# Kernel optimization log

Hardware: AMD Instinct MI355X
Metric: run time of the kernel (lower is better)

The kernel has to match this reference:

```python
import jax, jax.numpy as jnp
import numpy as np

B, LAT, H, F, L, NL = 128, 128, 512, 128, 256, 2


def setup_inputs() -> dict:
    key = jax.random.key(0)
    ks = jax.random.split(key, 20)
    s = 0.05  # keep recurrence well-conditioned
    def n(k, shp):
        return jax.random.normal(k, shp, dtype=jnp.float32) * s
    return dict(
        z=jax.random.normal(ks[0], (B, LAT), dtype=jnp.float32),
        W_l2h=n(ks[1], (H * NL, LAT)), b_l2h=n(ks[2], (H * NL,)),
        W_l2c=n(ks[3], (H * NL, LAT)), b_l2c=n(ks[4], (H * NL,)),
        W_zp=n(ks[5], (H, LAT)), b_zp=n(ks[6], (H,)),
        W_ih0=n(ks[7], (4 * H, F + H)), W_hh0=n(ks[8], (4 * H, H)),
        b_ih0=n(ks[9], (4 * H,)), b_hh0=n(ks[10], (4 * H,)),
        W_ih1=n(ks[11], (4 * H, H)), W_hh1=n(ks[12], (4 * H, H)),
        b_ih1=n(ks[13], (4 * H,)), b_hh1=n(ks[14], (4 * H,)),
        ln_g=jnp.ones((H,), jnp.float32), ln_b=jnp.zeros((H,), jnp.float32),
        W_pre=n(ks[15], (H, H)), b_pre=n(ks[16], (H,)),
        W_out=n(ks[17], (F, H)), b_out=n(ks[18], (F,)),
    )


def _lstm_cell(x, h, c, Wih, Whh, bih, bhh):
    # PyTorch gate order: i, f, g, o
    gates = x @ Wih.T + bih + h @ Whh.T + bhh
    i, f, g, o = jnp.split(gates, 4, axis=-1)
    c = jax.nn.sigmoid(f) * c + jax.nn.sigmoid(i) * jnp.tanh(g)
    h = jax.nn.sigmoid(o) * jnp.tanh(c)
    return h, c


def _layernorm(x, g, b, eps=1e-5):
    m = jnp.mean(x, axis=-1, keepdims=True)
    v = jnp.var(x, axis=-1, keepdims=True)
    return (x - m) * jax.lax.rsqrt(v + eps) * g + b


def reference(z, W_l2h, b_l2h, W_l2c, b_l2c, W_zp, b_zp,
              W_ih0, W_hh0, b_ih0, b_hh0, W_ih1, W_hh1, b_ih1, b_hh1,
              ln_g, ln_b, W_pre, b_pre, W_out, b_out):
    # Faithful to torch: (B, NL*H) viewed row-major as (NL, B, H)
    h0 = (z @ W_l2h.T + b_l2h).reshape(NL, B, H)
    c0 = (z @ W_l2c.T + b_l2c).reshape(NL, B, H)
    z_proj = z @ W_zp.T + b_zp  # (B, H), injected every step
    dec0 = jnp.zeros((B, F), dtype=z.dtype)

    def step(carry, _):
        ha, ca, hb, cb, dec = carry
        x = jnp.concatenate([dec, z_proj], axis=-1)  # (B, F+H)
        ha, ca = _lstm_cell(x, ha, ca, W_ih0, W_hh0, b_ih0, b_hh0)
        hb, cb = _lstm_cell(ha, hb, cb, W_ih1, W_hh1, b_ih1, b_hh1)
        ln = _layernorm(hb, ln_g, ln_b)
        pre = jax.nn.relu(ln @ W_pre.T + b_pre)
        out_t = (pre + ln) @ W_out.T + b_out  # residual through MLP
        return (ha, ca, hb, cb, out_t), out_t

    _, ys = jax.lax.scan(step, (h0[0], c0[0], h0[1], c0[1], dec0), None, length=L)
    return jnp.transpose(ys, (1, 0, 2))  # (B, L, F)
```

## Files before the change

### kernel.cpp

```cpp
#include <hip/hip_runtime.h>
#include <hip/hip_cooperative_groups.h>

namespace cg = cooperative_groups;


typedef unsigned int uint32;
typedef unsigned short u16;
typedef __attribute__((ext_vector_type(8))) short bf16x8;
typedef __attribute__((ext_vector_type(4))) float f32x4;

static constexpr int Ln = 256, Fn = 128;
static constexpr int APS = 65536;
static constexpr int WPS = 2097152;
static constexpr int OPS = 65536;
static constexpr int PPS = 262144;

static constexpr int BAR_WORDS = 4096;

static constexpr int ROWP = 520;
static constexpr int PLANE = 16 * ROWP;
static constexpr int SACT_ELEMS = 6 * PLANE;

static constexpr int SM_HV   = 0;
static constexpr int SM_LNH  = 33024;
static constexpr int SM_LNM  = 49664;
static constexpr int SM_LNL  = 66304;
static constexpr int SM_RED  = 82944;
static constexpr int SM_MEAN = 83968;
static constexpr int SM_RSTD = 84032;
static constexpr int SMEM_BYTES = 84096;

__device__ __forceinline__ u16 f2bf(float f) {
  union { float f; uint32 u; } v; v.f = f;
  uint32 u = v.u + 0x7fffu + ((v.u >> 16) & 1u);
  return (u16)(u >> 16);
}
__device__ __forceinline__ float bf2f(u16 h) {
  union { uint32 u; float f; } v; v.u = ((uint32)h) << 16;
  return v.f;
}
__device__ __forceinline__ void splitbf3(float v, u16* hi, u16* mid, u16* lo) {
  u16 h = f2bf(v);
  float r = v - bf2f(h);
  u16 m = f2bf(r);
  float r2 = r - bf2f(m);
  *hi = h; *mid = m; *lo = f2bf(r2);
}
__device__ __forceinline__ float sigm(float x) { return 1.f / (1.f + expf(-x)); }
__device__ __forceinline__ bf16x8 ldf(const u16* p) { return *(const bf16x8*)p; }

__device__ __forceinline__ bf16x8 ldc16(const u16* p) {
  bf16x8 r;
  asm volatile("global_load_dwordx4 %0, %1, off sc0 sc1" : "=v"(r) : "v"(p) : "memory");
  return r;
}
__device__ __forceinline__ void stc2(u16* p, u16 v) {
  asm volatile("global_store_short %0, %1, off sc0 sc1" :: "v"(p), "v"((uint32)v) : "memory");
}
__device__ __forceinline__ void vwait0_fence() {
  asm volatile("s_waitcnt vmcnt(0)" ::: "memory");
  __builtin_amdgcn_sched_barrier(0);
}

__device__ __forceinline__ void gbar_g(uint32* arr, uint32 ep, int blk) {
  asm volatile("s_waitcnt vmcnt(0) lgkmcnt(0)" ::: "memory");
  __syncthreads();
  int tid = threadIdx.x;
  if (tid == 0)
    __hip_atomic_store(&arr[blk * 16], ep, __ATOMIC_RELAXED, __HIP_MEMORY_SCOPE_AGENT);
  int base = (blk >> 5) << 5;
  for (;;) {
    uint32 v = (tid < 32)
        ? __hip_atomic_load(&arr[(base + tid) * 16], __ATOMIC_RELAXED, __HIP_MEMORY_SCOPE_AGENT)
        : ep;
    if (__syncthreads_and(v >= ep)) break;
    __builtin_amdgcn_s_sleep(1);
  }
  __builtin_amdgcn_sched_barrier(0);
}

#define MFMA1(A, B, ACC) ACC = __builtin_amdgcn_mfma_f32_16x16x32_bf16((A), (B), (ACC), 0, 0, 0)
#define MFMA6(AH, AM, AL, BH, BM, BL, A0, A1, A2) \
  do {                                            \
    MFMA1(AH, BH, A0);                            \
    MFMA1(AH, BM, A1); MFMA1(AM, BH, A1);         \
    MFMA1(AH, BL, A2); MFMA1(AL, BH, A2);         \
    MFMA1(AM, BM, A2);                            \
  } while (0)


__device__ __forceinline__ void stage_side(const u16* __restrict__ g, int b0,
                                           u16* sAct, int sideBase, int tid) {
  bf16x8 tv[12];
#pragma unroll
  for (int jr = 0; jr < 12; ++jr) {
    int plane = jr >> 2;
    int c2 = tid + ((jr & 3) << 8);
    int row = c2 >> 6, col = c2 & 63;
    tv[jr] = ldc16(g + (size_t)plane * APS + (size_t)(b0 + row) * 512 + col * 8);
  }
  vwait0_fence();
#pragma unroll
  for (int jr = 0; jr < 12; ++jr) {
    int plane = jr >> 2;
    int c2 = tid + ((jr & 3) << 8);
    int row = c2 >> 6, col = c2 & 63;
    *(bf16x8*)&sAct[sideBase + plane * PLANE + row * ROWP + col * 8] = tv[jr];
  }
}

__device__ __forceinline__ void gate_tile_p(
    const u16* __restrict__ g0, const u16* __restrict__ g1,
    const u16* __restrict__ wr,
    const float* __restrict__ bias, int bias_stride,
    float& cr, u16* __restrict__ hout,
    int b0, int h0, int tid, u16* sAct, float (*gbuf)[16][16]) {
  stage_side(g0, b0, sAct, 0, tid);
  stage_side(g1, b0, sAct, 3 * PLANE, tid);
  __syncthreads();
  int lane = tid & 63, w = tid >> 6, q = lane >> 4, r16 = lane & 15;
  const u16* aB = sAct + r16 * ROWP + q * 8;
  f32x4 A0 = {0.f, 0.f, 0.f, 0.f}, A1 = {0.f, 0.f, 0.f, 0.f}, A2 = {0.f, 0.f, 0.f, 0.f};
#pragma unroll
  for (int kb = 0; kb < 16; ++kb) {
    bf16x8 ah = ldf(aB + kb * 32), am = ldf(aB + PLANE + kb * 32), al = ldf(aB + 2 * PLANE + kb * 32);
    bf16x8 bh = ldf(wr + kb * 32), bm = ldf(wr + WPS + kb * 32), bl = ldf(wr + 2 * WPS + kb * 32);
    MFMA6(ah, am, al, bh, bm, bl, A0, A1, A2);
  }
#pragma unroll
  for (int kb = 0; kb < 16; ++kb) {
    bf16x8 ah = ldf(aB + 3 * PLANE + kb * 32), am = ldf(aB + 4 * PLANE + kb * 32),
           al = ldf(aB + 5 * PLANE + kb * 32);
    bf16x8 bh = ldf(wr + 512 + kb * 32), bm = ldf(wr + WPS + 512 + kb * 32),
           bl = ldf(wr + 2 * WPS + 512 + kb * 32);
    MFMA6(ah, am, al, bh, bm, bl, A0, A1, A2);
  }
#pragma unroll
  for (int r = 0; r < 4; ++r)
    gbuf[w][q * 4 + r][r16] = (A2[r] + A1[r]) + A0[r];
  __syncthreads();
  int bl_ = tid >> 4, hl = tid & 15;
  int b = b0 + bl_, h = h0 + hl;
  const float* bb = bias + (size_t)b * bias_stride;
  float gi = gbuf[0][bl_][hl] + bb[h];
  float gf = gbuf[1][bl_][hl] + bb[512 + h];
  float gc = gbuf[2][bl_][hl] + bb[1024 + h];
  float go = gbuf[3][bl_][hl] + bb[1536 + h];
  int idx = b * 512 + h;
  float cn = sigm(gf) * cr + sigm(gi) * tanhf(gc);
  cr = cn;
  float hv_ = sigm(go) * tanhf(cn);
  u16 hh, hm, hl2;
  splitbf3(hv_, &hh, &hm, &hl2);
  stc2(hout + idx, hh);
  stc2(hout + APS + idx, hm);
  stc2(hout + 2 * APS + idx, hl2);
}

__device__ __forceinline__ void ys_tile_p(
    const u16* __restrict__ sg, const u16* __restrict__ wr,
    const float* __restrict__ b_out, float* __restrict__ ys,
    int tout, int b0, int f0, int tid, u16* sAct) {
  stage_side(sg, b0, sAct, 0, tid);
  __syncthreads();
  int lane = tid & 63, q = lane >> 4, r16 = lane & 15;
  const u16* aB = sAct + r16 * ROWP + q * 8;
  f32x4 A0 = {0.f, 0.f, 0.f, 0.f}, A1 = {0.f, 0.f, 0.f, 0.f}, A2 = {0.f, 0.f, 0.f, 0.f};
#pragma unroll
  for (int kb = 0; kb < 16; ++kb) {
    bf16x8 ah = ldf(aB + kb * 32), am = ldf(aB + PLANE + kb * 32), al = ldf(aB + 2 * PLANE + kb * 32);
    bf16x8 bh = ldf(wr + kb * 32), bm = ldf(wr + OPS + kb * 32), bl = ldf(wr + 2 * OPS + kb * 32);
    MFMA6(ah, am, al, bh, bm, bl, A0, A1, A2);
  }
  int fc = f0 + r16;
  float bo = b_out[fc];
#pragma unroll
  for (int r = 0; r < 4; ++r) {
    int b = b0 + q * 4 + r;
    ys[(size_t)b * (Ln * Fn) + (size_t)tout * Fn + fc] = ((A2[r] + A1[r]) + A0[r]) + bo;
  }
}

__device__ __forceinline__ void lnpre_tile_p(
    const u16* __restrict__ hb, const u16* __restrict__ wr,
    const float* __restrict__ lng, const float* __restrict__ lnb,
    const float* __restrict__ b_pre, u16* __restrict__ s_out,
    int j0, int b0, int tid, char* smem) {
  float* hv = (float*)(smem + SM_HV);
  u16* lnH = (u16*)(smem + SM_LNH);
  u16* lnM = (u16*)(smem + SM_LNM);
  u16* lnL = (u16*)(smem + SM_LNL);
  float (*red)[16] = (float (*)[16])(smem + SM_RED);
  float* smean = (float*)(smem + SM_MEAN);
  float* srstd = (float*)(smem + SM_RSTD);
  bf16x8 p[12];
#pragma unroll
  for (int jj = 0; jj < 4; ++jj) {
    int c = tid + 256 * jj;
    int b = c >> 6, k0 = (c & 63) * 8;
    size_t base = (size_t)(b0 + b) * 512 + k0;
    p[jj * 3 + 0] = ldc16(hb + base);
    p[jj * 3 + 1] = ldc16(hb + APS + base);
    p[jj * 3 + 2] = ldc16(hb + 2 * APS + base);
  }
  vwait0_fence();
#pragma unroll
  for (int jj = 0; jj < 4; ++jj) {
    int c = tid + 256 * jj;
    int b = c >> 6, k0 = (c & 63) * 8;
#pragma unroll
    for (int e = 0; e < 8; ++e)
      hv[b * 516 + k0 + e] = (bf2f((u16)p[jj * 3 + 2][e]) + bf2f((u16)p[jj * 3 + 1][e])) +
                             bf2f((u16)p[jj * 3 + 0][e]);
  }
  __syncthreads();
  int bl_ = tid >> 4, kc = tid & 15;
  {
    float sm = 0.f;
    for (int kk = 0; kk < 32; ++kk) sm += hv[bl_ * 516 + kc * 32 + kk];
    red[bl_][kc] = sm;
  }
  __syncthreads();
  if (tid < 16) {
    float s1 = 0.f;
    for (int i = 0; i < 16; ++i) s1 += red[tid][i];
    smean[tid] = s1 * (1.f / 512.f);
  }
  __syncthreads();
  {
    float m = smean[bl_], sq = 0.f;
    for (int kk = 0; kk < 32; ++kk) {
      float d = hv[bl_ * 516 + kc * 32 + kk] - m;
      sq += d * d;
    }
    red[bl_][kc] = sq;
  }
  __syncthreads();
  if (tid < 16) {
    float s2 = 0.f;
    for (int i = 0; i < 16; ++i) s2 += red[tid][i];
    srstd[tid] = 1.f / sqrtf(s2 * (1.f / 512.f) + 1e-5f);
  }
  __syncthreads();
  for (int i = tid; i < 16 * 512; i += 256) {
    int b = i >> 9, k = i & 511;
    float v = (hv[b * 516 + k] - smean[b]) * srstd[b] * lng[k] + lnb[k];
    splitbf3(v, &lnH[b * 520 + k], &lnM[b * 520 + k], &lnL[b * 520 + k]);
  }
  __syncthreads();
  int lane = tid & 63, w = tid >> 6, q = lane >> 4, r16 = lane & 15;
  const u16* aH = lnH + r16 * 520 + q * 8;
  const u16* aM = lnM + r16 * 520 + q * 8;
  const u16* aL = lnL + r16 * 520 + q * 8;
  f32x4 A0 = {0.f, 0.f, 0.f, 0.f}, A1 = {0.f, 0.f, 0.f, 0.f}, A2 = {0.f, 0.f, 0.f, 0.f};
#pragma unroll
  for (int kb = 0; kb < 16; ++kb) {
    bf16x8 ah = ldf(aH + kb * 32), am = ldf(aM + kb * 32), al = ldf(aL + kb * 32);
    bf16x8 bh = ldf(wr + kb * 32), bm = ldf(wr + PPS + kb * 32), bl = ldf(wr + 2 * PPS + kb * 32);
    MFMA6(ah, am, al, bh, bm, bl, A0, A1, A2);
  }
  int j = j0 + w * 16 + r16;
  float bp = b_pre[j];
#pragma unroll
  for (int r = 0; r < 4; ++r) {
    int b = q * 4 + r;
    float lnv = (hv[b * 516 + j] - smean[b]) * srstd[b] * lng[j] + lnb[j];
    float pre = fmaxf(((A2[r] + A1[r]) + A0[r]) + bp, 0.f);
    float sval = pre + lnv;
    size_t sidx = (size_t)(b0 + b) * 512 + j;
    u16 sh, sm_, sl;
    splitbf3(sval, &sh, &sm_, &sl);
    stc2(s_out + sidx, sh);
    stc2(s_out + APS + sidx, sm_);
    stc2(s_out + 2 * APS + sidx, sl);
  }
}


__device__ __forceinline__ void gate_tile(
    const u16* __restrict__ a0, const u16* __restrict__ a1,
    const u16* __restrict__ wr,
    const float* __restrict__ bias, int bias_stride,
    float* __restrict__ cstate, u16* __restrict__ hout,
    int b0, int h0, int tid, float (*gbuf)[16][16]) {
  int w = tid >> 6;
  int lane = tid & 63, q = lane >> 4, r16 = lane & 15;
  f32x4 A0 = {0.f, 0.f, 0.f, 0.f}, A1 = {0.f, 0.f, 0.f, 0.f}, A2 = {0.f, 0.f, 0.f, 0.f};
#pragma unroll
  for (int kb = 0; kb < 16; ++kb) {
    bf16x8 ah = ldf(a0 + kb * 32), am = ldf(a0 + APS + kb * 32), al = ldf(a0 + 2 * APS + kb * 32);
    bf16x8 bh = ldf(wr + kb * 32), bm = ldf(wr + WPS + kb * 32), bl = ldf(wr + 2 * WPS + kb * 32);
    MFMA6(ah, am, al, bh, bm, bl, A0, A1, A2);
  }
#pragma unroll
  for (int kb = 0; kb < 16; ++kb) {
    bf16x8 ah = ldf(a1 + kb * 32), am = ldf(a1 + APS + kb * 32), al = ldf(a1 + 2 * APS + kb * 32);
    bf16x8 bh = ldf(wr + 512 + kb * 32), bm = ldf(wr + WPS + 512 + kb * 32),
           bl = ldf(wr + 2 * WPS + 512 + kb * 32);
    MFMA6(ah, am, al, bh, bm, bl, A0, A1, A2);
  }
#pragma unroll
  for (int r = 0; r < 4; ++r)
    gbuf[w][q * 4 + r][r16] = (A2[r] + A1[r]) + A0[r];
  __syncthreads();
  int bl_ = tid >> 4, hl = tid & 15;
  int b = b0 + bl_, h = h0 + hl;
  const float* bb = bias + (size_t)b * bias_stride;
  float gi = gbuf[0][bl_][hl] + bb[h];
  float gf = gbuf[1][bl_][hl] + bb[512 + h];
  float gc = gbuf[2][bl_][hl] + bb[1024 + h];
  float go = gbuf[3][bl_][hl] + bb[1536 + h];
  int idx = b * 512 + h;
  float c = cstate[idx];
  float cn = sigm(gf) * c + sigm(gi) * tanhf(gc);
  cstate[idx] = cn;
  float hv_ = sigm(go) * tanhf(cn);
  splitbf3(hv_, &hout[idx], &hout[APS + idx], &hout[2 * APS + idx]);
  __syncthreads();
}

__device__ __forceinline__ void ys_tile(
    const u16* __restrict__ a, const u16* __restrict__ wr,
    const float* __restrict__ b_out, float* __restrict__ ys,
    int tout, int b0, int f0, int tid) {
  int lane = tid & 63, q = lane >> 4, r16 = lane & 15;
  f32x4 A0 = {0.f, 0.f, 0.f, 0.f}, A1 = {0.f, 0.f, 0.f, 0.f}, A2 = {0.f, 0.f, 0.f, 0.f};
#pragma unroll
  for (int kb = 0; kb < 16; ++kb) {
    bf16x8 ah = ldf(a + kb * 32), am = ldf(a + APS + kb * 32), al = ldf(a + 2 * APS + kb * 32);
    bf16x8 bh = ldf(wr + kb * 32), bm = ldf(wr + OPS + kb * 32), bl = ldf(wr + 2 * OPS + kb * 32);
    MFMA6(ah, am, al, bh, bm, bl, A0, A1, A2);
  }
  int fc = f0 + r16;
  float bo = b_out[fc];
#pragma unroll
  for (int r = 0; r < 4; ++r) {
    int b = b0 + q * 4 + r;
    ys[(size_t)b * (Ln * Fn) + (size_t)tout * Fn + fc] = ((A2[r] + A1[r]) + A0[r]) + bo;
  }
}

__device__ __forceinline__ void lnpre_tile(
    const u16* __restrict__ hb, const u16* __restrict__ wr,
    const float* __restrict__ lng, const float* __restrict__ lnb,
    const float* __restrict__ b_pre, u16* __restrict__ s_out,
    int j0, int b0, int tid, char* smem) {
  float* hv = (float*)(smem + SM_HV);
  u16* lnH = (u16*)(smem + SM_LNH);
  u16* lnM = (u16*)(smem + SM_LNM);
  u16* lnL = (u16*)(smem + SM_LNL);
  float (*red)[16] = (float (*)[16])(smem + SM_RED);
  float* smean = (float*)(smem + SM_MEAN);
  float* srstd = (float*)(smem + SM_RSTD);
  for (int i = tid; i < 16 * 512; i += 256) {
    int b = i >> 9, k = i & 511;
    size_t hidx = (size_t)(b0 + b) * 512 + k;
    hv[b * 516 + k] = (bf2f(hb[2 * APS + hidx]) + bf2f(hb[APS + hidx])) + bf2f(hb[hidx]);
  }
  __syncthreads();
  int bl_ = tid >> 4, kc = tid & 15;
  {
    float sm = 0.f;
    for (int kk = 0; kk < 32; ++kk) sm += hv[bl_ * 516 + kc * 32 + kk];
    red[bl_][kc] = sm;
  }
  __syncthreads();
  if (tid < 16) {
    float s1 = 0.f;
    for (int i = 0; i < 16; ++i) s1 += red[tid][i];
    smean[tid] = s1 * (1.f / 512.f);
  }
  __syncthreads();
  {
    float m = smean[bl_], sq = 0.f;
    for (int kk = 0; kk < 32; ++kk) {
      float d = hv[bl_ * 516 + kc * 32 + kk] - m;
      sq += d * d;
    }
    red[bl_][kc] = sq;
  }
  __syncthreads();
  if (tid < 16) {
    float s2 = 0.f;
    for (int i = 0; i < 16; ++i) s2 += red[tid][i];
    srstd[tid] = 1.f / sqrtf(s2 * (1.f / 512.f) + 1e-5f);
  }
  __syncthreads();
  for (int i = tid; i < 16 * 512; i += 256) {
    int b = i >> 9, k = i & 511;
    float v = (hv[b * 516 + k] - smean[b]) * srstd[b] * lng[k] + lnb[k];
    splitbf3(v, &lnH[b * 520 + k], &lnM[b * 520 + k], &lnL[b * 520 + k]);
  }
  __syncthreads();
  int lane = tid & 63, w = tid >> 6, q = lane >> 4, r16 = lane & 15;
  const u16* aH = lnH + r16 * 520 + q * 8;
  const u16* aM = lnM + r16 * 520 + q * 8;
  const u16* aL = lnL + r16 * 520 + q * 8;
  f32x4 A0 = {0.f, 0.f, 0.f, 0.f}, A1 = {0.f, 0.f, 0.f, 0.f}, A2 = {0.f, 0.f, 0.f, 0.f};
#pragma unroll
  for (int kb = 0; kb < 16; ++kb) {
    bf16x8 ah = ldf(aH + kb * 32), am = ldf(aM + kb * 32), al = ldf(aL + kb * 32);
    bf16x8 bh = ldf(wr + kb * 32), bm = ldf(wr + PPS + kb * 32), bl = ldf(wr + 2 * PPS + kb * 32);
    MFMA6(ah, am, al, bh, bm, bl, A0, A1, A2);
  }
  int j = j0 + w * 16 + r16;
  float bp = b_pre[j];
#pragma unroll
  for (int r = 0; r < 4; ++r) {
    int b = q * 4 + r;
    float lnv = (hv[b * 516 + j] - smean[b]) * srstd[b] * lng[j] + lnb[j];
    float pre = fmaxf(((A2[r] + A1[r]) + A0[r]) + bp, 0.f);
    float sval = pre + lnv;
    size_t sidx = (size_t)(b0 + b) * 512 + j;
    splitbf3(sval, &s_out[sidx], &s_out[APS + sidx], &s_out[2 * APS + sidx]);
  }
  __syncthreads();
}


__global__ void prep_hc0(const float* __restrict__ z,
                         const float* __restrict__ W_l2h, const float* __restrict__ b_l2h,
                         const float* __restrict__ W_l2c, const float* __restrict__ b_l2c,
                         u16* __restrict__ ha0, u16* __restrict__ hb0,
                         float* __restrict__ ca, float* __restrict__ cb) {
  int idx = blockIdx.x * 256 + threadIdx.x;
  int b = idx & 127, j = idx >> 7;
  float ah = b_l2h[j], ac = b_l2c[j];
  for (int k = 0; k < 128; ++k) {
    float zv = z[b * 128 + k];
    ah += zv * W_l2h[j * 128 + k];
    ac += zv * W_l2c[j * 128 + k];
  }
  int flat = b * 1024 + j;
  if (flat < 65536) {
    splitbf3(ah, &ha0[flat], &ha0[APS + flat], &ha0[2 * APS + flat]);
    ca[flat] = ac;
  } else {
    flat -= 65536;
    splitbf3(ah, &hb0[flat], &hb0[APS + flat], &hb0[2 * APS + flat]);
    cb[flat] = ac;
  }
}

__global__ void prep_zp(const float* __restrict__ z, const float* __restrict__ W_zp,
                        const float* __restrict__ b_zp, float* __restrict__ zp) {
  int idx = blockIdx.x * 256 + threadIdx.x;
  int b = idx & 127, h = idx >> 7;
  float a = b_zp[h];
  for (int k = 0; k < 128; ++k) a += z[b * 128 + k] * W_zp[h * 128 + k];
  zp[b * 512 + h] = a;
}

__global__ void prep_gz(const float* __restrict__ zp, const float* __restrict__ W_ih0,
                        const float* __restrict__ b_ih0, const float* __restrict__ b_hh0,
                        const float* __restrict__ b_out,
                        float* __restrict__ GZ0, float* __restrict__ GZ1) {
  int idx = blockIdx.x * 256 + threadIdx.x;
  int b = idx & 127, g = idx >> 7;
  const float* wr = W_ih0 + (size_t)g * 640;
  float a = b_ih0[g] + b_hh0[g];
  for (int k = 0; k < 512; ++k) a += zp[b * 512 + k] * wr[128 + k];
  float co = 0.f;
  for (int f = 0; f < 128; ++f) co += b_out[f] * wr[f];
  GZ0[b * 2048 + g] = a;
  GZ1[b * 2048 + g] = a + co;
}

__global__ void prep_waf(const float* __restrict__ W_out, const float* __restrict__ W_ih0,
                         const float* __restrict__ W_hh0, u16* __restrict__ WAf) {
  int idx = blockIdx.x * 256 + threadIdx.x;
  int k = idx & 1023, g = idx >> 10;
  float v;
  if (k < 512) {
    v = 0.f;
    const float* wr = W_ih0 + (size_t)g * 640;
    for (int f = 0; f < 128; ++f) v += W_out[f * 512 + k] * wr[f];
  } else {
    v = W_hh0[(size_t)g * 512 + (k - 512)];
  }
  splitbf3(v, &WAf[idx], &WAf[WPS + idx], &WAf[2 * WPS + idx]);
}

__global__ void prep_wbf(const float* __restrict__ W_ih1, const float* __restrict__ W_hh1,
                         u16* __restrict__ WBf) {
  int idx = blockIdx.x * 256 + threadIdx.x;
  int k = idx & 1023, g = idx >> 10;
  float v = (k < 512) ? W_ih1[(size_t)g * 512 + k] : W_hh1[(size_t)g * 512 + (k - 512)];
  splitbf3(v, &WBf[idx], &WBf[WPS + idx], &WBf[2 * WPS + idx]);
}

__global__ void prep_misc(const float* __restrict__ W_pre, const float* __restrict__ W_out,
                          const float* __restrict__ b_ih1, const float* __restrict__ b_hh1,
                          u16* __restrict__ WPf, u16* __restrict__ WOf,
                          float* __restrict__ gb1, u16* __restrict__ s,
                          uint32* __restrict__ bar) {
  int idx = blockIdx.x * 256 + threadIdx.x;
  if (idx < 262144) { splitbf3(W_pre[idx], &WPf[idx], &WPf[PPS + idx], &WPf[2 * PPS + idx]); return; }
  idx -= 262144;
  if (idx < 65536) { splitbf3(W_out[idx], &WOf[idx], &WOf[OPS + idx], &WOf[2 * OPS + idx]); return; }
  idx -= 65536;
  if (idx < 2048) { gb1[idx] = b_ih1[idx] + b_hh1[idx]; return; }
  idx -= 2048;
  if (idx < 196608) { s[idx] = 0; return; }
  idx -= 196608;
  if (idx < BAR_WORDS) bar[idx] = 0;
}


__global__ __launch_bounds__(256, 1) void loop_k(
    const u16* __restrict__ WAf, const u16* __restrict__ WBf,
    const u16* __restrict__ WPf, const u16* __restrict__ WOf,
    const float* __restrict__ GZ0, const float* __restrict__ GZ1,
    const float* __restrict__ gb1,
    const float* __restrict__ ca, const float* __restrict__ cb,
    u16* __restrict__ ha0, u16* __restrict__ ha1,
    u16* __restrict__ hb0, u16* __restrict__ hb1,
    u16* __restrict__ s0, u16* __restrict__ s1,
    const float* __restrict__ lng, const float* __restrict__ lnb,
    const float* __restrict__ b_pre, const float* __restrict__ b_out,
    float* __restrict__ ys, uint32* __restrict__ bar) {
  __shared__ __align__(16) u16 sAct[SACT_ELEMS];
  __shared__ float gbuf[4][16][16];
  int tid = threadIdx.x;
  int lane = tid & 63, w = tid >> 6, q = lane >> 4, r16 = lane & 15;
  int blk = blockIdx.x;

  int gg = blk & 31, bg = blk >> 5;
  int h0A = gg * 16, b0A = bg * 16;
  size_t wro = (size_t)(w * 512 + h0A + r16) * 1024 + q * 8;
  const u16* wrA = WAf + wro;
  const u16* wrB = WBf + wro;

  int j0 = gg * 64;
  const u16* wrP = WPf + (size_t)(j0 + w * 16 + r16) * 512 + q * 8;
  int fh = gg & 1;
  int f0 = fh * 64 + w * 16;
  const u16* wrO = WOf + (size_t)(f0 + r16) * 512 + q * 8;

  int cidx = (b0A + (tid >> 4)) * 512 + h0A + (tid & 15);
  float cA = ca[cidx], cB = cb[cidx];

  uint32 ep = 0;
  for (int t = 0; t < Ln; ++t) {
    u16* sPrev = (t & 1) ? s0 : s1;
    u16* sNext = (t & 1) ? s1 : s0;
    u16* haIn  = (t & 1) ? ha1 : ha0;
    u16* haOut = (t & 1) ? ha0 : ha1;
    u16* hbIn  = (t & 1) ? hb1 : hb0;
    u16* hbOut = (t & 1) ? hb0 : hb1;

    gate_tile_p(sPrev, haIn, wrA, t ? GZ1 : GZ0, 2048, cA, haOut, b0A, h0A, tid, sAct, gbuf);
    gbar_g(bar, ++ep, blk);
    gate_tile_p(haOut, hbIn, wrB, gb1, 0, cB, hbOut, b0A, h0A, tid, sAct, gbuf);
    gbar_g(bar, ++ep, blk);
    if (gg < 8) {
      lnpre_tile_p(hbOut, wrP, lng, lnb, b_pre, sNext, j0, b0A, tid, (char*)sAct);
    } else if (gg < 10 && t > 0) {
      ys_tile_p(sPrev, wrO, b_out, ys, t - 1, b0A, f0, tid, sAct);
    }
    gbar_g(bar, ++ep, blk);
  }
  if (gg >= 8 && gg < 10) {
    ys_tile_p(s1, wrO, b_out, ys, Ln - 1, b0A, f0, tid, sAct);
  }
}


__global__ void cell_k(const u16* __restrict__ x0, const u16* __restrict__ x1,
                       const u16* __restrict__ Wf,
                       const float* __restrict__ bias, int bias_stride,
                       float* __restrict__ cstate, u16* __restrict__ hout,
                       int n_gate_blocks,
                       const u16* sv, const u16* __restrict__ WOf,
                       const float* __restrict__ b_out, float* __restrict__ ys, int t) {
  __shared__ float gbuf[4][16][16];
  int tid = threadIdx.x;
  int lane = tid & 63, w = tid >> 6, q = lane >> 4, r16 = lane & 15;
  int blk = blockIdx.x;
  if (blk < n_gate_blocks) {
    int gg = blk & 31, bg = blk >> 5;
    int h0 = gg * 16, b0 = bg * 16;
    const u16* wr = Wf + (size_t)(w * 512 + h0 + r16) * 1024 + q * 8;
    size_t aoff = (size_t)(b0 + r16) * 512 + q * 8;
    gate_tile(x0 + aoff, x1 + aoff, wr, bias, bias_stride, cstate, hout, b0, h0, tid, gbuf);
  } else {
    if (t < 1) return;
    int ob = blk - n_gate_blocks;
    int bg = ob >> 1, fh = ob & 1;
    int b0 = bg * 16, f0 = fh * 64 + w * 16;
    const u16* wr = WOf + (size_t)(f0 + r16) * 512 + q * 8;
    size_t aoff = (size_t)(b0 + r16) * 512 + q * 8;
    ys_tile(sv + aoff, wr, b_out, ys, t - 1, b0, f0, tid);
  }
}

__global__ void lnpre_k(const u16* __restrict__ hb, const u16* __restrict__ WPf,
                        const float* __restrict__ lng, const float* __restrict__ lnb,
                        const float* __restrict__ b_pre, u16* __restrict__ s_out) {
  __shared__ __align__(16) char smem[SMEM_BYTES];
  int tid = threadIdx.x;
  int lane = tid & 63, w = tid >> 6, q = lane >> 4, r16 = lane & 15;
  int jg = blockIdx.x & 7, bg = blockIdx.x >> 3;
  int j0 = jg * 64, b0 = bg * 16;
  const u16* wr = WPf + (size_t)(j0 + w * 16 + r16) * 512 + q * 8;
  lnpre_tile(hb, wr, lng, lnb, b_pre, s_out, j0, b0, tid, smem);
}


extern "C" void kernel_launch(void* const* d_in, const int* in_sizes, int n_in,
                              void* d_out, int out_size, void* d_ws, size_t ws_size,
                              hipStream_t stream) {
  const float* z     = (const float*)d_in[0];
  const float* W_l2h = (const float*)d_in[1];
  const float* b_l2h = (const float*)d_in[2];
  const float* W_l2c = (const float*)d_in[3];
  const float* b_l2c = (const float*)d_in[4];
  const float* W_zp  = (const float*)d_in[5];
  const float* b_zp  = (const float*)d_in[6];
  const float* W_ih0 = (const float*)d_in[7];
  const float* W_hh0 = (const float*)d_in[8];
  const float* b_ih0 = (const float*)d_in[9];
  const float* b_hh0 = (const float*)d_in[10];
  const float* W_ih1 = (const float*)d_in[11];
  const float* W_hh1 = (const float*)d_in[12];
  const float* b_ih1 = (const float*)d_in[13];
  const float* b_hh1 = (const float*)d_in[14];
  const float* ln_g  = (const float*)d_in[15];
  const float* ln_b  = (const float*)d_in[16];
  const float* W_pre = (const float*)d_in[17];
  const float* b_pre = (const float*)d_in[18];
  const float* W_out = (const float*)d_in[19];
  const float* b_out = (const float*)d_in[20];
  float* out = (float*)d_out;
  char* ws = (char*)d_ws;

  size_t off = 0;
  auto alloc = [&](size_t bytes) { void* p = ws + off; off += bytes; return p; };
  u16*   WAf  = (u16*)alloc(12582912);
  u16*   WBf  = (u16*)alloc(12582912);
  u16*   WPf  = (u16*)alloc(1572864);
  u16*   WOf  = (u16*)alloc(393216);
  float* GZ0  = (float*)alloc(1048576);
  float* GZ1  = (float*)alloc(1048576);
  float* gb1  = (float*)alloc(8192);
  float* zp   = (float*)alloc(262144);
  u16*   ha[2], *hbuf[2], *sb[2];
  ha[0]   = (u16*)alloc(393216);
  ha[1]   = (u16*)alloc(393216);
  hbuf[0] = (u16*)alloc(393216);
  hbuf[1] = (u16*)alloc(393216);
  float* ca   = (float*)alloc(262144);
  float* cb   = (float*)alloc(262144);
  sb[0]   = (u16*)alloc(393216);
  sb[1]   = (u16*)alloc(393216);
  uint32* bar = (uint32*)alloc(32768);

  prep_hc0<<<512, 256, 0, stream>>>(z, W_l2h, b_l2h, W_l2c, b_l2c, ha[0], hbuf[0], ca, cb);
  prep_zp<<<256, 256, 0, stream>>>(z, W_zp, b_zp, zp);
  prep_gz<<<1024, 256, 0, stream>>>(zp, W_ih0, b_ih0, b_hh0, b_out, GZ0, GZ1);
  prep_waf<<<8192, 256, 0, stream>>>(W_out, W_ih0, W_hh0, WAf);
  prep_wbf<<<8192, 256, 0, stream>>>(W_ih1, W_hh1, WBf);
  prep_misc<<<2073, 256, 0, stream>>>(W_pre, W_out, b_ih1, b_hh1, WPf, WOf, gb1, sb[1], bar);

  static int coop_supported = -1;
  if (coop_supported < 0) {
    int dev = 0;
    (void)hipGetDevice(&dev);
    int v = 0;
    (void)hipDeviceGetAttribute(&v, hipDeviceAttributeCooperativeLaunch, dev);
    coop_supported = v;
  }

  bool did_coop = false;
  if (coop_supported) {
    void* kargs[] = {
        (void*)&WAf, (void*)&WBf, (void*)&WPf, (void*)&WOf,
        (void*)&GZ0, (void*)&GZ1, (void*)&gb1, (void*)&ca, (void*)&cb,
        (void*)&ha[0], (void*)&ha[1], (void*)&hbuf[0], (void*)&hbuf[1],
        (void*)&sb[0], (void*)&sb[1],
        (void*)&ln_g, (void*)&ln_b, (void*)&b_pre, (void*)&b_out, (void*)&out,
        (void*)&bar};
    hipError_t err = hipLaunchCooperativeKernel((const void*)loop_k, dim3(256), dim3(256),
                                                kargs, 0, stream);
    did_coop = (err == hipSuccess);
  }

  if (!did_coop) {
    for (int t = 0; t < Ln; ++t) {
      u16* sPrev = (t & 1) ? sb[0] : sb[1];
      u16* sNext = (t & 1) ? sb[1] : sb[0];
      u16* haIn = ha[t & 1];
      u16* haOut = ha[(t + 1) & 1];
      u16* hbIn = hbuf[t & 1];
      u16* hbOut = hbuf[(t + 1) & 1];
      cell_k<<<272, 256, 0, stream>>>(sPrev, haIn, WAf, t ? GZ1 : GZ0, 2048,
                                      ca, haOut, 256, sPrev, WOf, b_out, out, t);
      cell_k<<<256, 256, 0, stream>>>(haOut, hbIn, WBf, gb1, 0,
                                      cb, hbOut, 256, sPrev, WOf, b_out, out, 0);
      lnpre_k<<<64, 256, 0, stream>>>(hbOut, WPf, ln_g, ln_b, b_pre, sNext);
    }
    cell_k<<<16, 256, 0, stream>>>(sb[1], ha[0], WAf, GZ1, 2048, ca, ha[1],
                                   0, sb[1], WOf, b_out, out, Ln);
  }
}
```

Baseline: 14.95 ms.

## Double block width to 512 threads, split gate K across waves, vectorize h stores

The persistent cooperative kernel now runs 512 threads per block. Waves 0-3 and 4-7 each compute half of the K dimension (input side versus recurrent side) of the gate GEMM, and the partial sums are added through shared memory. The hidden-state and LN-pre outputs are first collected in a shared tile and then written with 16-byte global stores instead of 2-byte scalar stores. The LN/pre and output projection work is redistributed to fewer blocks with wider tiles, and the barrier spin loop now has an iteration cap and a longer sleep. This is meant to shorten the serial MFMA chain per step and cut store transactions, at the cost of extra block syncs and a barrier that could exit before all blocks have arrived.

```diff
diff --git a/kernel.cpp b/kernel.cpp
--- a/kernel.cpp
+++ b/kernel.cpp
@@ -19,7 +19,9 @@
 
 static constexpr int ROWP = 520;
 static constexpr int PLANE = 16 * ROWP;
-static constexpr int SACT_ELEMS = 6 * PLANE;
+static constexpr int SM_GBUF  = 99840;
+static constexpr int SM_HTILE = 108032;
+static constexpr int SMEM_TOTAL = 109568;
 
 static constexpr int SM_HV   = 0;
 static constexpr int SM_LNH  = 33024;
@@ -54,8 +56,8 @@
   asm volatile("global_load_dwordx4 %0, %1, off sc0 sc1" : "=v"(r) : "v"(p) : "memory");
   return r;
 }
-__device__ __forceinline__ void stc2(u16* p, u16 v) {
-  asm volatile("global_store_short %0, %1, off sc0 sc1" :: "v"(p), "v"((uint32)v) : "memory");
+__device__ __forceinline__ void stc16(u16* p, bf16x8 v) {
+  asm volatile("global_store_dwordx4 %0, %1, off sc0 sc1" :: "v"(p), "v"(v) : "memory");
 }
 __device__ __forceinline__ void vwait0_fence() {
   asm volatile("s_waitcnt vmcnt(0)" ::: "memory");
@@ -69,12 +71,12 @@
   if (tid == 0)
     __hip_atomic_store(&arr[blk * 16], ep, __ATOMIC_RELAXED, __HIP_MEMORY_SCOPE_AGENT);
   int base = (blk >> 5) << 5;
-  for (;;) {
+  for (int spin = 0; spin < (1 << 18); ++spin) {
     uint32 v = (tid < 32)
         ? __hip_atomic_load(&arr[(base + tid) * 16], __ATOMIC_RELAXED, __HIP_MEMORY_SCOPE_AGENT)
         : ep;
     if (__syncthreads_and(v >= ep)) break;
-    __builtin_amdgcn_s_sleep(1);
+    __builtin_amdgcn_s_sleep(2);
   }
   __builtin_amdgcn_sched_barrier(0);
 }
@@ -89,37 +91,66 @@
   } while (0)
 
 
-__device__ __forceinline__ void stage_side(const u16* __restrict__ g, int b0,
-                                           u16* sAct, int sideBase, int tid) {
+__device__ __forceinline__ void stage2(const u16* __restrict__ g0,
+                                       const u16* __restrict__ g1,
+                                       int b0, u16* sAct, int tid) {
   bf16x8 tv[12];
 #pragma unroll
   for (int jr = 0; jr < 12; ++jr) {
-    int plane = jr >> 2;
-    int c2 = tid + ((jr & 3) << 8);
-    int row = c2 >> 6, col = c2 & 63;
+    int c = tid + (jr << 9);
+    int side = c / 3072;
+    int rem = c - side * 3072;
+    int plane = rem >> 10, rem2 = rem & 1023;
+    int row = rem2 >> 6, col = rem2 & 63;
+    const u16* gp = side ? g1 : g0;
+    tv[jr] = ldc16(gp + (size_t)plane * APS + (size_t)(b0 + row) * 512 + col * 8);
+  }
+  vwait0_fence();
+#pragma unroll
+  for (int jr = 0; jr < 12; ++jr) {
+    int c = tid + (jr << 9);
+    int side = c / 3072;
+    int rem = c - side * 3072;
+    int plane = rem >> 10, rem2 = rem & 1023;
+    int row = rem2 >> 6, col = rem2 & 63;
+    *(bf16x8*)&sAct[side * 3 * PLANE + plane * PLANE + row * ROWP + col * 8] = tv[jr];
+  }
+}
+
+__device__ __forceinline__ void stage1(const u16* __restrict__ g,
+                                       int b0, u16* sAct, int tid) {
+  bf16x8 tv[6];
+#pragma unroll
+  for (int jr = 0; jr < 6; ++jr) {
+    int c = tid + (jr << 9);
+    int plane = c >> 10, rem2 = c & 1023;
+    int row = rem2 >> 6, col = rem2 & 63;
     tv[jr] = ldc16(g + (size_t)plane * APS + (size_t)(b0 + row) * 512 + col * 8);
   }
   vwait0_fence();
 #pragma unroll
-  for (int jr = 0; jr < 12; ++jr) {
-    int plane = jr >> 2;
-    int c2 = tid + ((jr & 3) << 8);
-    int row = c2 >> 6, col = c2 & 63;
-    *(bf16x8*)&sAct[sideBase + plane * PLANE + row * ROWP + col * 8] = tv[jr];
-  }
-}
-
-__device__ __forceinline__ void gate_tile_p(
+  for (int jr = 0; jr < 6; ++jr) {
+    int c = tid + (jr << 9);
+    int plane = c >> 10, rem2 = c & 1023;
+    int row = rem2 >> 6, col = rem2 & 63;
+    *(bf16x8*)&sAct[plane * PLANE + row * ROWP + col * 8] = tv[jr];
+  }
+}
+
+__device__ __forceinline__ void gate_tile_p2(
     const u16* __restrict__ g0, const u16* __restrict__ g1,
     const u16* __restrict__ wr,
     const float* __restrict__ bias, int bias_stride,
     float& cr, u16* __restrict__ hout,
-    int b0, int h0, int tid, u16* sAct, float (*gbuf)[16][16]) {
-  stage_side(g0, b0, sAct, 0, tid);
-  stage_side(g1, b0, sAct, 3 * PLANE, tid);
+    int b0, int h0, int tid, char* smem) {
+  u16* sAct = (u16*)smem;
+  float (*gbuf)[16][16] = (float (*)[16][16])(smem + SM_GBUF);
+  u16* htile = (u16*)(smem + SM_HTILE);
+  stage2(g0, g1, b0, sAct, tid);
   __syncthreads();
   int lane = tid & 63, w = tid >> 6, q = lane >> 4, r16 = lane & 15;
-  const u16* aB = sAct + r16 * ROWP + q * 8;
+  int side = w >> 2;
+  const u16* aB = sAct + side * 3 * PLANE + r16 * ROWP + q * 8;
   f32x4 A0 = {0.f, 0.f, 0.f, 0.f}, A1 = {0.f, 0.f, 0.f, 0.f}, A2 = {0.f, 0.f, 0.f, 0.f};
 #pragma unroll
   for (int kb = 0; kb < 16; ++kb) {
@@ -128,42 +159,42 @@
     MFMA6(ah, am, al, bh, bm, bl, A0, A1, A2);
   }
 #pragma unroll
-  for (int kb = 0; kb < 16; ++kb) {
-    bf16x8 ah = ldf(aB + 3 * PLANE + kb * 32), am = ldf(aB + 4 * PLANE + kb * 32),
-           al = ldf(aB + 5 * PLANE + kb * 32);
-    bf16x8 bh = ldf(wr + 512 + kb * 32), bm = ldf(wr + WPS + 512 + kb * 32),
-           bl = ldf(wr + 2 * WPS + 512 + kb * 32);
-    MFMA6(ah, am, al, bh, bm, bl, A0, A1, A2);
-  }
-#pragma unroll
   for (int r = 0; r < 4; ++r)
     gbuf[w][q * 4 + r][r16] = (A2[r] + A1[r]) + A0[r];
   __syncthreads();
-  int bl_ = tid >> 4, hl = tid & 15;
-  int b = b0 + bl_, h = h0 + hl;
-  const float* bb = bias + (size_t)b * bias_stride;
-  float gi = gbuf[0][bl_][hl] + bb[h];
-  float gf = gbuf[1][bl_][hl] + bb[512 + h];
-  float gc = gbuf[2][bl_][hl] + bb[1024 + h];
-  float go = gbuf[3][bl_][hl] + bb[1536 + h];
-  int idx = b * 512 + h;
-  float cn = sigm(gf) * cr + sigm(gi) * tanhf(gc);
-  cr = cn;
-  float hv_ = sigm(go) * tanhf(cn);
-  u16 hh, hm, hl2;
-  splitbf3(hv_, &hh, &hm, &hl2);
-  stc2(hout + idx, hh);
-  stc2(hout + APS + idx, hm);
-  stc2(hout + 2 * APS + idx, hl2);
-}
-
-__device__ __forceinline__ void ys_tile_p(
+  if (tid < 256) {
+    int bl_ = tid >> 4, hl = tid & 15;
+    int b = b0 + bl_, h = h0 + hl;
+    const float* bb = bias + (size_t)b * bias_stride;
+    float gi = (gbuf[0][bl_][hl] + gbuf[4][bl_][hl]) + bb[h];
+    float gf = (gbuf[1][bl_][hl] + gbuf[5][bl_][hl]) + bb[512 + h];
+    float gc = (gbuf[2][bl_][hl] + gbuf[6][bl_][hl]) + bb[1024 + h];
+    float go = (gbuf[3][bl_][hl] + gbuf[7][bl_][hl]) + bb[1536 + h];
+    float cn = sigm(gf) * cr + sigm(gi) * tanhf(gc);
+    cr = cn;
+    float hv_ = sigm(go) * tanhf(cn);
+    u16 hh, hm, hl2;
+    splitbf3(hv_, &hh, &hm, &hl2);
+    htile[(0 * 16 + bl_) * 16 + hl] = hh;
+    htile[(1 * 16 + bl_) * 16 + hl] = hm;
+    htile[(2 * 16 + bl_) * 16 + hl] = hl2;
+  }
+  __syncthreads();
+  if (tid < 96) {
+    int p = tid >> 5, seg = tid & 31, row = seg >> 1, half = seg & 1;
+    bf16x8 v = *(bf16x8*)&htile[(p * 16 + row) * 16 + half * 8];
+    stc16(hout + (size_t)p * APS + (size_t)(b0 + row) * 512 + h0 + half * 8, v);
+  }
+}
+
+__device__ __forceinline__ void ys_tile_p2(
     const u16* __restrict__ sg, const u16* __restrict__ wr,
     const float* __restrict__ b_out, float* __restrict__ ys,
-    int tout, int b0, int f0, int tid, u16* sAct) {
-  stage_side(sg, b0, sAct, 0, tid);
-  __syncthreads();
-  int lane = tid & 63, q = lane >> 4, r16 = lane & 15;
+    int tout, int b0, int tid, char* smem) {
+  u16* sAct = (u16*)smem;
+  stage1(sg, b0, sAct, tid);
+  __syncthreads();
+  int lane = tid & 63, w = tid >> 6, q = lane >> 4, r16 = lane & 15;
   const u16* aB = sAct + r16 * ROWP + q * 8;
   f32x4 A0 = {0.f, 0.f, 0.f, 0.f}, A1 = {0.f, 0.f, 0.f, 0.f}, A2 = {0.f, 0.f, 0.f, 0.f};
 #pragma unroll
@@ -172,7 +203,7 @@
     bf16x8 bh = ldf(wr + kb * 32), bm = ldf(wr + OPS + kb * 32), bl = ldf(wr + 2 * OPS + kb * 32);
     MFMA6(ah, am, al, bh, bm, bl, A0, A1, A2);
   }
-  int fc = f0 + r16;
+  int fc = w * 16 + r16;
   float bo = b_out[fc];
 #pragma unroll
   for (int r = 0; r < 4; ++r) {
@@ -181,7 +212,7 @@
   }
 }
 
-__device__ __forceinline__ void lnpre_tile_p(
+__device__ __forceinline__ void lnpre_tile_p2(
     const u16* __restrict__ hb, const u16* __restrict__ wr,
     const float* __restrict__ lng, const float* __restrict__ lnb,
     const float* __restrict__ b_pre, u16* __restrict__ s_out,
@@ -193,10 +224,10 @@
   float (*red)[16] = (float (*)[16])(smem + SM_RED);
   float* smean = (float*)(smem + SM_MEAN);
   float* srstd = (float*)(smem + SM_RSTD);
-  bf16x8 p[12];
-#pragma unroll
-  for (int jj = 0; jj < 4; ++jj) {
-    int c = tid + 256 * jj;
+  bf16x8 p[6];
+#pragma unroll
+  for (int jj = 0; jj < 2; ++jj) {
+    int c = tid + (jj << 9);
     int b = c >> 6, k0 = (c & 63) * 8;
     size_t base = (size_t)(b0 + b) * 512 + k0;
     p[jj * 3 + 0] = ldc16(hb + base);
@@ -205,8 +236,8 @@
   }
   vwait0_fence();
 #pragma unroll
-  for (int jj = 0; jj < 4; ++jj) {
-    int c = tid + 256 * jj;
+  for (int jj = 0; jj < 2; ++jj) {
+    int c = tid + (jj << 9);
     int b = c >> 6, k0 = (c & 63) * 8;
 #pragma unroll
     for (int e = 0; e < 8; ++e)
@@ -214,8 +245,8 @@
                              bf2f((u16)p[jj * 3 + 0][e]);
   }
   __syncthreads();
-  int bl_ = tid >> 4, kc = tid & 15;
-  {
+  if (tid < 256) {
+    int bl_ = tid >> 4, kc = tid & 15;
     float sm = 0.f;
     for (int kk = 0; kk < 32; ++kk) sm += hv[bl_ * 516 + kc * 32 + kk];
     red[bl_][kc] = sm;
@@ -227,7 +258,8 @@
     smean[tid] = s1 * (1.f / 512.f);
   }
   __syncthreads();
-  {
+  if (tid < 256) {
+    int bl_ = tid >> 4, kc = tid & 15;
     float m = smean[bl_], sq = 0.f;
     for (int kk = 0; kk < 32; ++kk) {
       float d = hv[bl_ * 516 + kc * 32 + kk] - m;
@@ -242,7 +274,7 @@
     srstd[tid] = 1.f / sqrtf(s2 * (1.f / 512.f) + 1e-5f);
   }
   __syncthreads();
-  for (int i = tid; i < 16 * 512; i += 256) {
+  for (int i = tid; i < 16 * 512; i += 512) {
     int b = i >> 9, k = i & 511;
     float v = (hv[b * 516 + k] - smean[b]) * srstd[b] * lng[k] + lnb[k];
     splitbf3(v, &lnH[b * 520 + k], &lnM[b * 520 + k], &lnL[b * 520 + k]);
@@ -259,7 +291,10 @@
     bf16x8 bh = ldf(wr + kb * 32), bm = ldf(wr + PPS + kb * 32), bl = ldf(wr + 2 * PPS + kb * 32);
     MFMA6(ah, am, al, bh, bm, bl, A0, A1, A2);
   }
+  __syncthreads();
+  u16* stile = (u16*)(smem + SM_LNH);
   int j = j0 + w * 16 + r16;
+  int jj = j - j0;
   float bp = b_pre[j];
 #pragma unroll
   for (int r = 0; r < 4; ++r) {
@@ -267,12 +302,17 @@
     float lnv = (hv[b * 516 + j] - smean[b]) * srstd[b] * lng[j] + lnb[j];
     float pre = fmaxf(((A2[r] + A1[r]) + A0[r]) + bp, 0.f);
     float sval = pre + lnv;
-    size_t sidx = (size_t)(b0 + b) * 512 + j;
     u16 sh, sm_, sl;
     splitbf3(sval, &sh, &sm_, &sl);
-    stc2(s_out + sidx, sh);
-    stc2(s_out + APS + sidx, sm_);
-    stc2(s_out + 2 * APS + sidx, sl);
+    stile[0 * 2048 + b * 128 + jj] = sh;
+    stile[1 * 2048 + b * 128 + jj] = sm_;
+    stile[2 * 2048 + b * 128 + jj] = sl;
+  }
+  __syncthreads();
+  for (int i = tid; i < 768; i += 512) {
+    int pl = i >> 8, rem = i & 255, b = rem >> 4, hs = rem & 15;
+    bf16x8 v = *(bf16x8*)&stile[pl * 2048 + b * 128 + hs * 8];
+    stc16(s_out + (size_t)pl * APS + (size_t)(b0 + b) * 512 + j0 + hs * 8, v);
   }
 }
 
@@ -507,7 +547,7 @@
 }
 
 
-__global__ __launch_bounds__(256, 1) void loop_k(
+__global__ __launch_bounds__(512, 2) void loop_k(
     const u16* __restrict__ WAf, const u16* __restrict__ WBf,
     const u16* __restrict__ WPf, const u16* __restrict__ WOf,
     const float* __restrict__ GZ0, const float* __restrict__ GZ1,
@@ -519,25 +559,24 @@
     const float* __restrict__ lng, const float* __restrict__ lnb,
     const float* __restrict__ b_pre, const float* __restrict__ b_out,
     float* __restrict__ ys, uint32* __restrict__ bar) {
-  __shared__ __align__(16) u16 sAct[SACT_ELEMS];
-  __shared__ float gbuf[4][16][16];
+  __shared__ __align__(16) char smem[SMEM_TOTAL];
   int tid = threadIdx.x;
   int lane = tid & 63, w = tid >> 6, q = lane >> 4, r16 = lane & 15;
   int blk = blockIdx.x;
 
   int gg = blk & 31, bg = blk >> 5;
   int h0A = gg * 16, b0A = bg * 16;
-  size_t wro = (size_t)(w * 512 + h0A + r16) * 1024 + q * 8;
+  int gate = w & 3, side = w >> 2;
+  size_t wro = (size_t)(gate * 512 + h0A + r16) * 1024 + side * 512 + q * 8;
   const u16* wrA = WAf + wro;
   const u16* wrB = WBf + wro;
 
-  int j0 = gg * 64;
-  const u16* wrP = WPf + (size_t)(j0 + w * 16 + r16) * 512 + q * 8;
-  int fh = gg & 1;
-  int f0 = fh * 64 + w * 16;
-  const u16* wrO = WOf + (size_t)(f0 + r16) * 512 + q * 8;
-
-  int cidx = (b0A + (tid >> 4)) * 512 + h0A + (tid & 15);
+  int j0C = (gg & 3) * 128;
+  const u16* wrP = WPf + (size_t)(j0C + w * 16 + r16) * 512 + q * 8;
+  const u16* wrO = WOf + (size_t)(w * 16 + r16) * 512 + q * 8;
+
+  int ct = tid & 255;
+  int cidx = (b0A + (ct >> 4)) * 512 + h0A + (ct & 15);
   float cA = ca[cidx], cB = cb[cidx];
 
   uint32 ep = 0;
@@ -549,19 +588,19 @@
     u16* hbIn  = (t & 1) ? hb1 : hb0;
     u16* hbOut = (t & 1) ? hb0 : hb1;
 
-    gate_tile_p(sPrev, haIn, wrA, t ? GZ1 : GZ0, 2048, cA, haOut, b0A, h0A, tid, sAct, gbuf);
+    gate_tile_p2(sPrev, haIn, wrA, t ? GZ1 : GZ0, 2048, cA, haOut, b0A, h0A, tid, smem);
     gbar_g(bar, ++ep, blk);
-    gate_tile_p(haOut, hbIn, wrB, gb1, 0, cB, hbOut, b0A, h0A, tid, sAct, gbuf);
+    gate_tile_p2(haOut, hbIn, wrB, gb1, 0, cB, hbOut, b0A, h0A, tid, smem);
     gbar_g(bar, ++ep, blk);
-    if (gg < 8) {
-      lnpre_tile_p(hbOut, wrP, lng, lnb, b_pre, sNext, j0, b0A, tid, (char*)sAct);
-    } else if (gg < 10 && t > 0) {
-      ys_tile_p(sPrev, wrO, b_out, ys, t - 1, b0A, f0, tid, sAct);
+    if (gg < 4) {
+      lnpre_tile_p2(hbOut, wrP, lng, lnb, b_pre, sNext, j0C, b0A, tid, smem);
+    } else if (gg == 4 && t > 0) {
+      ys_tile_p2(sPrev, wrO, b_out, ys, t - 1, b0A, tid, smem);
     }
     gbar_g(bar, ++ep, blk);
   }
-  if (gg >= 8 && gg < 10) {
-    ys_tile_p(s1, wrO, b_out, ys, Ln - 1, b0A, f0, tid, sAct);
+  if (gg == 4) {
+    ys_tile_p2(s1, wrO, b_out, ys, Ln - 1, b0A, tid, smem);
   }
 }
 
@@ -680,7 +719,7 @@
         (void*)&sb[0], (void*)&sb[1],
         (void*)&ln_g, (void*)&ln_b, (void*)&b_pre, (void*)&b_out, (void*)&out,
         (void*)&bar};
-    hipError_t err = hipLaunchCooperativeKernel((const void*)loop_k, dim3(256), dim3(256),
+    hipError_t err = hipLaunchCooperativeKernel((const void*)loop_k, dim3(256), dim3(512),
                                                 kargs, 0, stream);
     did_coop = (err == hipSuccess);
   }
```

After: 14.98 ms. Within noise of the previous version (+0.2%).
